# Kernel optimization log

Measured on AMD Instinct MI355X. Metric: run time of the kernel, lower is better.

## Reference

```python
import jax, jax.numpy as jnp
import numpy as np

N_NODES = 100000
D = 128            # hidden_size*2
N_EDGES = 1600000  # avg degree 16
NUM_LABELS = 1024


def setup_inputs() -> dict:
    key = jax.random.key(0)
    ks = jax.random.split(key, 16)
    inputs = jax.random.normal(ks[0], (N_NODES, D), dtype=jnp.float32)
    src = jax.random.randint(ks[1], (N_EDGES,), 0, N_NODES, dtype=jnp.int64)
    dst = jax.random.randint(ks[2], (N_EDGES,), 0, N_NODES, dtype=jnp.int64)
    s = 0.05
    # GIN layer 1 (conv linear) + residual block 1
    eps1 = jnp.zeros((), dtype=jnp.float32)
    W1 = jax.random.normal(ks[3], (D, D), dtype=jnp.float32) * s
    b1 = jnp.zeros((D,), dtype=jnp.float32)
    rW1 = jax.random.normal(ks[4], (D, D), dtype=jnp.float32) * s
    rb1 = jnp.zeros((D,), dtype=jnp.float32)
    # GIN layer 2 + residual block 2
    eps2 = jnp.zeros((), dtype=jnp.float32)
    W2 = jax.random.normal(ks[5], (D, D), dtype=jnp.float32) * s
    b2 = jnp.zeros((D,), dtype=jnp.float32)
    rW2 = jax.random.normal(ks[6], (D, D), dtype=jnp.float32) * s
    rb2 = jnp.zeros((D,), dtype=jnp.float32)
    # final multi-label head
    linW = jax.random.normal(ks[7], (D, NUM_LABELS), dtype=jnp.float32) * s
    linb = jnp.zeros((NUM_LABELS,), dtype=jnp.float32)
    return dict(inputs=inputs, src=src, dst=dst,
                eps1=eps1, W1=W1, b1=b1, rW1=rW1, rb1=rb1,
                eps2=eps2, W2=W2, b2=b2, rW2=rW2, rb2=rb2,
                linW=linW, linb=linb)


def reference(inputs, src, dst, eps1, W1, b1, rW1, rb1,
              eps2, W2, b2, rW2, rb2, linW, linb):
    n = inputs.shape[0]

    def gin_conv(h, eps, W, b):
        # sum-aggregate neighbor features: irregular gather + scatter-add
        agg = jax.ops.segment_sum(h[src], dst, num_segments=n)  # [N, D]
        return ((1.0 + eps) * h + agg) @ W + b

    def residual_block(h, rW, rb):
        # Sequential(ReLU, Dropout(eval=identity), Residual(D, D))
        h = jax.nn.relu(h)
        return h + jax.nn.relu(h @ rW + rb)

    h1 = residual_block(gin_conv(inputs, eps1, W1, b1), rW1, rb1)
    h2 = residual_block(gin_conv(h1, eps2, W2, b2), rW2, rb2)

    stacked = jnp.stack([h1, h2], axis=1)   # [N, n_layers, D] == stack_embed
    pooled = stacked.mean(axis=1)           # [N, D]
    return pooled @ linW + linb             # [N, NUM_LABELS]
```

## Files before the change

### kernel.cpp

```cpp
#include <hip/hip_runtime.h>

#define DIM 128
#define NLAB 1024
#define MT 64
#define LDK 136

typedef __bf16 bf16x4 __attribute__((ext_vector_type(4)));
typedef __bf16 bf16x8 __attribute__((ext_vector_type(8)));
typedef float  f32x4  __attribute__((ext_vector_type(4)));

__global__ __launch_bounds__(256) void k_hist(
    const int* __restrict__ dst, int* __restrict__ cnt, int nE) {
  int e = blockIdx.x * 256 + threadIdx.x;
  if (e < nE) atomicAdd(&cnt[dst[e]], 1);
}

__global__ __launch_bounds__(1024) void k_scan(
    const int* __restrict__ cnt, int* __restrict__ off,
    int* __restrict__ cur, int n) {
  __shared__ int part[1024];
  const int t = threadIdx.x;
  const int per = (n + 1023) >> 10;
  const int start = t * per;
  const int end = min(start + per, n);
  int s = 0;
  for (int i = start; i < end; ++i) s += cnt[i];
  part[t] = s;
  __syncthreads();
  for (int d = 1; d < 1024; d <<= 1) {
    int v = (t >= d) ? part[t - d] : 0;
    __syncthreads();
    part[t] += v;
    __syncthreads();
  }
  int excl = (t == 0) ? 0 : part[t - 1];
  if (t == 1023) off[n] = part[1023];
  for (int i = start; i < end; ++i) {
    int c = cnt[i];
    off[i] = excl;
    cur[i] = excl;
    excl += c;
  }
}

__global__ __launch_bounds__(256) void k_binfill(
    const int* __restrict__ src, const int* __restrict__ dst,
    int* __restrict__ cur, int* __restrict__ eidx, int nE) {
  int e = blockIdx.x * 256 + threadIdx.x;
  if (e < nE) {
    int p = atomicAdd(&cur[dst[e]], 1);
    eidx[p] = src[e];
  }
}

__global__ __launch_bounds__(256) void k_gather(
    const float* __restrict__ h, const int* __restrict__ off,
    const int* __restrict__ eidx, float* __restrict__ agg, int n) {
  int node = blockIdx.x * 8 + (threadIdx.x >> 5);
  if (node >= n) return;
  int c = (threadIdx.x & 31) << 2;
  int beg = off[node], end = off[node + 1];
  float4 a0 = make_float4(0.f, 0.f, 0.f, 0.f);
  float4 a1 = a0, a2 = a0, a3 = a0;
  int e = beg;
  for (; e + 4 <= end; e += 4) {
    int s0 = eidx[e + 0];
    int s1 = eidx[e + 1];
    int s2 = eidx[e + 2];
    int s3 = eidx[e + 3];
    float4 v0 = *(const float4*)(h + (size_t)s0 * DIM + c);
    float4 v1 = *(const float4*)(h + (size_t)s1 * DIM + c);
    float4 v2 = *(const float4*)(h + (size_t)s2 * DIM + c);
    float4 v3 = *(const float4*)(h + (size_t)s3 * DIM + c);
    a0.x += v0.x; a0.y += v0.y; a0.z += v0.z; a0.w += v0.w;
    a1.x += v1.x; a1.y += v1.y; a1.z += v1.z; a1.w += v1.w;
    a2.x += v2.x; a2.y += v2.y; a2.z += v2.z; a2.w += v2.w;
    a3.x += v3.x; a3.y += v3.y; a3.z += v3.z; a3.w += v3.w;
  }
  for (; e < end; ++e) {
    int s = eidx[e];
    float4 v = *(const float4*)(h + (size_t)s * DIM + c);
    a0.x += v.x; a0.y += v.y; a0.z += v.z; a0.w += v.w;
  }
  a0.x += a1.x + a2.x + a3.x;
  a0.y += a1.y + a2.y + a3.y;
  a0.z += a1.z + a2.z + a3.z;
  a0.w += a1.w + a2.w + a3.w;
  *(float4*)(agg + (size_t)node * DIM + c) = a0;
}

__global__ __launch_bounds__(256) void k_gin_conv(
    const float* __restrict__ hin, const float* __restrict__ agg,
    const float* __restrict__ epsp, const float* __restrict__ W,
    const float* __restrict__ bias, float* __restrict__ hout, int n) {
  __shared__ __bf16 As[MT][LDK];
  __shared__ __bf16 Bs[DIM][LDK];
  const int t = threadIdx.x;
  const int rowBase = blockIdx.x * MT;
  const float e1 = 1.0f + epsp[0];

#pragma unroll
  for (int it = 0; it < 8; ++it) {
    int idx = (it * 256 + t) << 2;
    int r = idx >> 7, c = idx & 127;
    int node = rowBase + r;
    float4 a4 = make_float4(0.f, 0.f, 0.f, 0.f);
    float4 g4 = a4;
    if (node < n) {
      a4 = *(const float4*)(hin + (size_t)node * DIM + c);
      g4 = *(const float4*)(agg + (size_t)node * DIM + c);
    }
    bf16x4 v;
    v[0] = (__bf16)(e1 * a4.x + g4.x);
    v[1] = (__bf16)(e1 * a4.y + g4.y);
    v[2] = (__bf16)(e1 * a4.z + g4.z);
    v[3] = (__bf16)(e1 * a4.w + g4.w);
    *(bf16x4*)&As[r][c] = v;
  }
  {
    int nloc = t & 127;
    int kh = (t >> 7) << 6;
#pragma unroll
    for (int kk = 0; kk < 64; ++kk) {
      int k = kh + kk;
      Bs[nloc][k] = (__bf16)W[(size_t)k * DIM + nloc];
    }
  }
  __syncthreads();

  const int wv = t >> 6, lane = t & 63;
  const int quad = lane >> 4, l16 = lane & 15;
  f32x4 acc[4][2];
#pragma unroll
  for (int i = 0; i < 4; ++i) {
    acc[i][0] = f32x4{0.f, 0.f, 0.f, 0.f};
    acc[i][1] = f32x4{0.f, 0.f, 0.f, 0.f};
  }

#pragma unroll
  for (int kc = 0; kc < 4; ++kc) {
    int kb = kc * 32 + quad * 8;
    bf16x8 b0 = *(const bf16x8*)&Bs[wv * 32 + l16][kb];
    bf16x8 b1 = *(const bf16x8*)&Bs[wv * 32 + 16 + l16][kb];
#pragma unroll
    for (int rt = 0; rt < 4; ++rt) {
      bf16x8 a = *(const bf16x8*)&As[rt * 16 + l16][kb];
      acc[rt][0] = __builtin_amdgcn_mfma_f32_16x16x32_bf16(a, b0, acc[rt][0], 0, 0, 0);
      acc[rt][1] = __builtin_amdgcn_mfma_f32_16x16x32_bf16(a, b1, acc[rt][1], 0, 0, 0);
    }
  }

#pragma unroll
  for (int rt = 0; rt < 4; ++rt) {
#pragma unroll
    for (int ct = 0; ct < 2; ++ct) {
      int ncol = wv * 32 + ct * 16 + l16;
      float bv = bias[ncol];
#pragma unroll
      for (int r = 0; r < 4; ++r) {
        int node = rowBase + rt * 16 + quad * 4 + r;
        if (node < n) {
          float v = acc[rt][ct][r] + bv;
          hout[(size_t)node * DIM + ncol] = fmaxf(v, 0.f);
        }
      }
    }
  }
}

__global__ __launch_bounds__(256) void k_residual(
    const float* __restrict__ hmid, const float* __restrict__ W,
    const float* __restrict__ bias, float* __restrict__ hout, int n) {
  __shared__ __bf16 As[MT][LDK];
  __shared__ __bf16 Bs[DIM][LDK];
  const int t = threadIdx.x;
  const int rowBase = blockIdx.x * MT;

#pragma unroll
  for (int it = 0; it < 8; ++it) {
    int idx = (it * 256 + t) << 2;
    int r = idx >> 7, c = idx & 127;
    int node = rowBase + r;
    float4 a4 = make_float4(0.f, 0.f, 0.f, 0.f);
    if (node < n) a4 = *(const float4*)(hmid + (size_t)node * DIM + c);
    bf16x4 v;
    v[0] = (__bf16)a4.x;
    v[1] = (__bf16)a4.y;
    v[2] = (__bf16)a4.z;
    v[3] = (__bf16)a4.w;
    *(bf16x4*)&As[r][c] = v;
  }
  {
    int nloc = t & 127;
    int kh = (t >> 7) << 6;
#pragma unroll
    for (int kk = 0; kk < 64; ++kk) {
      int k = kh + kk;
      Bs[nloc][k] = (__bf16)W[(size_t)k * DIM + nloc];
    }
  }
  __syncthreads();

  const int wv = t >> 6, lane = t & 63;
  const int quad = lane >> 4, l16 = lane & 15;
  f32x4 acc[4][2];
#pragma unroll
  for (int i = 0; i < 4; ++i) {
    acc[i][0] = f32x4{0.f, 0.f, 0.f, 0.f};
    acc[i][1] = f32x4{0.f, 0.f, 0.f, 0.f};
  }

#pragma unroll
  for (int kc = 0; kc < 4; ++kc) {
    int kb = kc * 32 + quad * 8;
    bf16x8 b0 = *(const bf16x8*)&Bs[wv * 32 + l16][kb];
    bf16x8 b1 = *(const bf16x8*)&Bs[wv * 32 + 16 + l16][kb];
#pragma unroll
    for (int rt = 0; rt < 4; ++rt) {
      bf16x8 a = *(const bf16x8*)&As[rt * 16 + l16][kb];
      acc[rt][0] = __builtin_amdgcn_mfma_f32_16x16x32_bf16(a, b0, acc[rt][0], 0, 0, 0);
      acc[rt][1] = __builtin_amdgcn_mfma_f32_16x16x32_bf16(a, b1, acc[rt][1], 0, 0, 0);
    }
  }

#pragma unroll
  for (int rt = 0; rt < 4; ++rt) {
#pragma unroll
    for (int ct = 0; ct < 2; ++ct) {
      int ncol = wv * 32 + ct * 16 + l16;
      float bv = bias[ncol];
#pragma unroll
      for (int r = 0; r < 4; ++r) {
        int node = rowBase + rt * 16 + quad * 4 + r;
        if (node < n) {
          float hv = hmid[(size_t)node * DIM + ncol];
          float v = fmaxf(acc[rt][ct][r] + bv, 0.f);
          hout[(size_t)node * DIM + ncol] = hv + v;
        }
      }
    }
  }
}

__global__ __launch_bounds__(256) void k_final(
    const float* __restrict__ h1, const float* __restrict__ h2,
    const float* __restrict__ W, const float* __restrict__ bias,
    float* __restrict__ out, int n) {
  __shared__ __bf16 As[MT][LDK];
  __shared__ __bf16 Bs[DIM][LDK];
  const int t = threadIdx.x;
  const int rowBase = blockIdx.x * MT;
  const int nb = blockIdx.y << 7;

#pragma unroll
  for (int it = 0; it < 8; ++it) {
    int idx = (it * 256 + t) << 2;
    int r = idx >> 7, c = idx & 127;
    int node = rowBase + r;
    float4 a4 = make_float4(0.f, 0.f, 0.f, 0.f);
    float4 b4 = a4;
    if (node < n) {
      a4 = *(const float4*)(h1 + (size_t)node * DIM + c);
      b4 = *(const float4*)(h2 + (size_t)node * DIM + c);
    }
    bf16x4 v;
    v[0] = (__bf16)(0.5f * (a4.x + b4.x));
    v[1] = (__bf16)(0.5f * (a4.y + b4.y));
    v[2] = (__bf16)(0.5f * (a4.z + b4.z));
    v[3] = (__bf16)(0.5f * (a4.w + b4.w));
    *(bf16x4*)&As[r][c] = v;
  }
  {
    int nloc = t & 127;
    int kh = (t >> 7) << 6;
#pragma unroll
    for (int kk = 0; kk < 64; ++kk) {
      int k = kh + kk;
      Bs[nloc][k] = (__bf16)W[(size_t)k * NLAB + nb + nloc];
    }
  }
  __syncthreads();

  const int wv = t >> 6, lane = t & 63;
  const int quad = lane >> 4, l16 = lane & 15;
  f32x4 acc[4][2];
#pragma unroll
  for (int i = 0; i < 4; ++i) {
    acc[i][0] = f32x4{0.f, 0.f, 0.f, 0.f};
    acc[i][1] = f32x4{0.f, 0.f, 0.f, 0.f};
  }

#pragma unroll
  for (int kc = 0; kc < 4; ++kc) {
    int kb = kc * 32 + quad * 8;
    bf16x8 b0 = *(const bf16x8*)&Bs[wv * 32 + l16][kb];
    bf16x8 b1 = *(const bf16x8*)&Bs[wv * 32 + 16 + l16][kb];
#pragma unroll
    for (int rt = 0; rt < 4; ++rt) {
      bf16x8 a = *(const bf16x8*)&As[rt * 16 + l16][kb];
      acc[rt][0] = __builtin_amdgcn_mfma_f32_16x16x32_bf16(a, b0, acc[rt][0], 0, 0, 0);
      acc[rt][1] = __builtin_amdgcn_mfma_f32_16x16x32_bf16(a, b1, acc[rt][1], 0, 0, 0);
    }
  }

#pragma unroll
  for (int rt = 0; rt < 4; ++rt) {
#pragma unroll
    for (int ct = 0; ct < 2; ++ct) {
      int ncol = wv * 32 + ct * 16 + l16;
      float bv = bias[nb + ncol];
#pragma unroll
      for (int r = 0; r < 4; ++r) {
        int node = rowBase + rt * 16 + quad * 4 + r;
        if (node < n) {
          out[(size_t)node * NLAB + nb + ncol] = acc[rt][ct][r] + bv;
        }
      }
    }
  }
}

extern "C" void kernel_launch(void* const* d_in, const int* in_sizes, int n_in,
                              void* d_out, int out_size, void* d_ws, size_t ws_size,
                              hipStream_t stream) {
  const float* inputs = (const float*)d_in[0];
  const int*   src    = (const int*)d_in[1];
  const int*   dst    = (const int*)d_in[2];
  const float* eps1   = (const float*)d_in[3];
  const float* W1     = (const float*)d_in[4];
  const float* b1     = (const float*)d_in[5];
  const float* rW1    = (const float*)d_in[6];
  const float* rb1    = (const float*)d_in[7];
  const float* eps2   = (const float*)d_in[8];
  const float* W2     = (const float*)d_in[9];
  const float* b2     = (const float*)d_in[10];
  const float* rW2    = (const float*)d_in[11];
  const float* rb2    = (const float*)d_in[12];
  const float* linW   = (const float*)d_in[13];
  const float* linb   = (const float*)d_in[14];
  float* out = (float*)d_out;

  const int n = in_sizes[0] / DIM;
  const int E = in_sizes[1];
  const size_t bufB = (size_t)n * DIM * sizeof(float);

  float* agg  = (float*)d_ws;
  float* hmid = (float*)((char*)d_ws + bufB);
  float* h1   = (float*)((char*)d_ws + 2 * bufB);
  float* h2   = agg;

  int* eidx = (int*)d_out;
  int* off  = eidx + E;
  int* cur  = off + (n + 1);

  const int rowBlocks = (n + MT - 1) / MT;
  const int eBlocks = (E + 255) / 256;
  const int gBlocks = (n + 7) / 8;
  dim3 fgrid(rowBlocks, NLAB / DIM);

  hipMemsetAsync(cur, 0, (size_t)n * sizeof(int), stream);
  k_hist<<<eBlocks, 256, 0, stream>>>(dst, cur, E);
  k_scan<<<1, 1024, 0, stream>>>(cur, off, cur, n);
  k_binfill<<<eBlocks, 256, 0, stream>>>(src, dst, cur, eidx, E);

  k_gather<<<gBlocks, 256, 0, stream>>>(inputs, off, eidx, agg, n);
  k_gin_conv<<<rowBlocks, 256, 0, stream>>>(inputs, agg, eps1, W1, b1, hmid, n);
  k_residual<<<rowBlocks, 256, 0, stream>>>(hmid, rW1, rb1, h1, n);
  k_gather<<<gBlocks, 256, 0, stream>>>(h1, off, eidx, agg, n);
  k_gin_conv<<<rowBlocks, 256, 0, stream>>>(h1, agg, eps2, W2, b2, hmid, n);
  k_residual<<<rowBlocks, 256, 0, stream>>>(hmid, rW2, rb2, h2, n);
  k_final<<<fgrid, 256, 0, stream>>>(h1, h2, linW, linb, out, n);
}
```

Before: 1.387 ms.

## Fuse GIN conv with residual block and fold final head into layer 2

Merges the GIN conv matmul and the residual matmul into one kernel per layer. The intermediate activation stays in registers and LDS instead of a round trip through global memory. Layer 2 also computes the mean of h1 and h2 and loops over all 8 label tiles of the head inside the same block, so h2 is never written. This removes several full-size N×128 reads and writes plus launches. The cost is that each block now loads linW 8 times serially and the final head has less parallelism (one block per row tile instead of 8).

```diff
diff --git a/kernel.cpp b/kernel.cpp
--- a/kernel.cpp
+++ b/kernel.cpp
@@ -89,16 +89,12 @@
   *(float4*)(agg + (size_t)node * DIM + c) = a0;
 }
 
-__global__ __launch_bounds__(256) void k_gin_conv(
-    const float* __restrict__ hin, const float* __restrict__ agg,
-    const float* __restrict__ epsp, const float* __restrict__ W,
-    const float* __restrict__ bias, float* __restrict__ hout, int n) {
-  __shared__ __bf16 As[MT][LDK];
-  __shared__ __bf16 Bs[DIM][LDK];
-  const int t = threadIdx.x;
-  const int rowBase = blockIdx.x * MT;
-  const float e1 = 1.0f + epsp[0];
-
+__device__ __forceinline__ void conv_residual_tile(
+    const float* __restrict__ hin, const float* __restrict__ agg, float e1,
+    const float* __restrict__ W, const float* __restrict__ bias,
+    const float* __restrict__ rW, const float* __restrict__ rbias,
+    __bf16 (*As)[LDK], __bf16 (*Bs)[LDK],
+    int rowBase, int n, int t, float ho[4][2][4]) {
 #pragma unroll
   for (int it = 0; it < 8; ++it) {
     int idx = (it * 256 + t) << 2;
@@ -136,7 +132,6 @@
     acc[i][0] = f32x4{0.f, 0.f, 0.f, 0.f};
     acc[i][1] = f32x4{0.f, 0.f, 0.f, 0.f};
   }
-
 #pragma unroll
   for (int kc = 0; kc < 4; ++kc) {
     int kb = kc * 32 + quad * 8;
@@ -150,173 +145,172 @@
     }
   }
 
-#pragma unroll
-  for (int rt = 0; rt < 4; ++rt) {
-#pragma unroll
-    for (int ct = 0; ct < 2; ++ct) {
-      int ncol = wv * 32 + ct * 16 + l16;
-      float bv = bias[ncol];
-#pragma unroll
-      for (int r = 0; r < 4; ++r) {
-        int node = rowBase + rt * 16 + quad * 4 + r;
-        if (node < n) {
-          float v = acc[rt][ct][r] + bv;
-          hout[(size_t)node * DIM + ncol] = fmaxf(v, 0.f);
-        }
-      }
-    }
-  }
-}
-
-__global__ __launch_bounds__(256) void k_residual(
-    const float* __restrict__ hmid, const float* __restrict__ W,
-    const float* __restrict__ bias, float* __restrict__ hout, int n) {
+  float hm[4][2][4];
+#pragma unroll
+  for (int rt = 0; rt < 4; ++rt)
+#pragma unroll
+    for (int ct = 0; ct < 2; ++ct) {
+      float bv = bias[wv * 32 + ct * 16 + l16];
+#pragma unroll
+      for (int r = 0; r < 4; ++r)
+        hm[rt][ct][r] = fmaxf(acc[rt][ct][r] + bv, 0.f);
+    }
+
+  __syncthreads();
+
+#pragma unroll
+  for (int rt = 0; rt < 4; ++rt)
+#pragma unroll
+    for (int ct = 0; ct < 2; ++ct) {
+      int col = wv * 32 + ct * 16 + l16;
+#pragma unroll
+      for (int r = 0; r < 4; ++r)
+        As[rt * 16 + quad * 4 + r][col] = (__bf16)hm[rt][ct][r];
+    }
+  {
+    int nloc = t & 127;
+    int kh = (t >> 7) << 6;
+#pragma unroll
+    for (int kk = 0; kk < 64; ++kk) {
+      int k = kh + kk;
+      Bs[nloc][k] = (__bf16)rW[(size_t)k * DIM + nloc];
+    }
+  }
+  __syncthreads();
+
+#pragma unroll
+  for (int i = 0; i < 4; ++i) {
+    acc[i][0] = f32x4{0.f, 0.f, 0.f, 0.f};
+    acc[i][1] = f32x4{0.f, 0.f, 0.f, 0.f};
+  }
+#pragma unroll
+  for (int kc = 0; kc < 4; ++kc) {
+    int kb = kc * 32 + quad * 8;
+    bf16x8 b0 = *(const bf16x8*)&Bs[wv * 32 + l16][kb];
+    bf16x8 b1 = *(const bf16x8*)&Bs[wv * 32 + 16 + l16][kb];
+#pragma unroll
+    for (int rt = 0; rt < 4; ++rt) {
+      bf16x8 a = *(const bf16x8*)&As[rt * 16 + l16][kb];
+      acc[rt][0] = __builtin_amdgcn_mfma_f32_16x16x32_bf16(a, b0, acc[rt][0], 0, 0, 0);
+      acc[rt][1] = __builtin_amdgcn_mfma_f32_16x16x32_bf16(a, b1, acc[rt][1], 0, 0, 0);
+    }
+  }
+
+#pragma unroll
+  for (int rt = 0; rt < 4; ++rt)
+#pragma unroll
+    for (int ct = 0; ct < 2; ++ct) {
+      float bv = rbias[wv * 32 + ct * 16 + l16];
+#pragma unroll
+      for (int r = 0; r < 4; ++r)
+        ho[rt][ct][r] = hm[rt][ct][r] + fmaxf(acc[rt][ct][r] + bv, 0.f);
+    }
+}
+
+__global__ __launch_bounds__(256) void k_layer1(
+    const float* __restrict__ hin, const float* __restrict__ agg,
+    const float* __restrict__ epsp, const float* __restrict__ W,
+    const float* __restrict__ bias, const float* __restrict__ rW,
+    const float* __restrict__ rbias, float* __restrict__ h1, int n) {
   __shared__ __bf16 As[MT][LDK];
   __shared__ __bf16 Bs[DIM][LDK];
   const int t = threadIdx.x;
   const int rowBase = blockIdx.x * MT;
-
-#pragma unroll
-  for (int it = 0; it < 8; ++it) {
-    int idx = (it * 256 + t) << 2;
-    int r = idx >> 7, c = idx & 127;
-    int node = rowBase + r;
-    float4 a4 = make_float4(0.f, 0.f, 0.f, 0.f);
-    if (node < n) a4 = *(const float4*)(hmid + (size_t)node * DIM + c);
-    bf16x4 v;
-    v[0] = (__bf16)a4.x;
-    v[1] = (__bf16)a4.y;
-    v[2] = (__bf16)a4.z;
-    v[3] = (__bf16)a4.w;
-    *(bf16x4*)&As[r][c] = v;
-  }
-  {
-    int nloc = t & 127;
-    int kh = (t >> 7) << 6;
-#pragma unroll
-    for (int kk = 0; kk < 64; ++kk) {
-      int k = kh + kk;
-      Bs[nloc][k] = (__bf16)W[(size_t)k * DIM + nloc];
-    }
-  }
-  __syncthreads();
-
+  float ho[4][2][4];
+  conv_residual_tile(hin, agg, 1.0f + epsp[0], W, bias, rW, rbias,
+                     As, Bs, rowBase, n, t, ho);
   const int wv = t >> 6, lane = t & 63;
   const int quad = lane >> 4, l16 = lane & 15;
-  f32x4 acc[4][2];
-#pragma unroll
-  for (int i = 0; i < 4; ++i) {
-    acc[i][0] = f32x4{0.f, 0.f, 0.f, 0.f};
-    acc[i][1] = f32x4{0.f, 0.f, 0.f, 0.f};
-  }
-
-#pragma unroll
-  for (int kc = 0; kc < 4; ++kc) {
-    int kb = kc * 32 + quad * 8;
-    bf16x8 b0 = *(const bf16x8*)&Bs[wv * 32 + l16][kb];
-    bf16x8 b1 = *(const bf16x8*)&Bs[wv * 32 + 16 + l16][kb];
-#pragma unroll
-    for (int rt = 0; rt < 4; ++rt) {
-      bf16x8 a = *(const bf16x8*)&As[rt * 16 + l16][kb];
-      acc[rt][0] = __builtin_amdgcn_mfma_f32_16x16x32_bf16(a, b0, acc[rt][0], 0, 0, 0);
-      acc[rt][1] = __builtin_amdgcn_mfma_f32_16x16x32_bf16(a, b1, acc[rt][1], 0, 0, 0);
-    }
-  }
-
-#pragma unroll
-  for (int rt = 0; rt < 4; ++rt) {
+#pragma unroll
+  for (int rt = 0; rt < 4; ++rt)
 #pragma unroll
     for (int ct = 0; ct < 2; ++ct) {
       int ncol = wv * 32 + ct * 16 + l16;
-      float bv = bias[ncol];
 #pragma unroll
       for (int r = 0; r < 4; ++r) {
         int node = rowBase + rt * 16 + quad * 4 + r;
-        if (node < n) {
-          float hv = hmid[(size_t)node * DIM + ncol];
-          float v = fmaxf(acc[rt][ct][r] + bv, 0.f);
-          hout[(size_t)node * DIM + ncol] = hv + v;
-        }
-      }
-    }
-  }
-}
-
-__global__ __launch_bounds__(256) void k_final(
-    const float* __restrict__ h1, const float* __restrict__ h2,
-    const float* __restrict__ W, const float* __restrict__ bias,
-    float* __restrict__ out, int n) {
+        if (node < n) h1[(size_t)node * DIM + ncol] = ho[rt][ct][r];
+      }
+    }
+}
+
+__global__ __launch_bounds__(256) void k_layer2f(
+    const float* __restrict__ h1, const float* __restrict__ agg,
+    const float* __restrict__ epsp, const float* __restrict__ W,
+    const float* __restrict__ bias, const float* __restrict__ rW,
+    const float* __restrict__ rbias, const float* __restrict__ linW,
+    const float* __restrict__ linb, float* __restrict__ out, int n) {
   __shared__ __bf16 As[MT][LDK];
   __shared__ __bf16 Bs[DIM][LDK];
   const int t = threadIdx.x;
   const int rowBase = blockIdx.x * MT;
-  const int nb = blockIdx.y << 7;
-
-#pragma unroll
-  for (int it = 0; it < 8; ++it) {
-    int idx = (it * 256 + t) << 2;
-    int r = idx >> 7, c = idx & 127;
-    int node = rowBase + r;
-    float4 a4 = make_float4(0.f, 0.f, 0.f, 0.f);
-    float4 b4 = a4;
-    if (node < n) {
-      a4 = *(const float4*)(h1 + (size_t)node * DIM + c);
-      b4 = *(const float4*)(h2 + (size_t)node * DIM + c);
-    }
-    bf16x4 v;
-    v[0] = (__bf16)(0.5f * (a4.x + b4.x));
-    v[1] = (__bf16)(0.5f * (a4.y + b4.y));
-    v[2] = (__bf16)(0.5f * (a4.z + b4.z));
-    v[3] = (__bf16)(0.5f * (a4.w + b4.w));
-    *(bf16x4*)&As[r][c] = v;
-  }
-  {
-    int nloc = t & 127;
-    int kh = (t >> 7) << 6;
-#pragma unroll
-    for (int kk = 0; kk < 64; ++kk) {
-      int k = kh + kk;
-      Bs[nloc][k] = (__bf16)W[(size_t)k * NLAB + nb + nloc];
-    }
-  }
-  __syncthreads();
-
+  float ho[4][2][4];
+  conv_residual_tile(h1, agg, 1.0f + epsp[0], W, bias, rW, rbias,
+                     As, Bs, rowBase, n, t, ho);
   const int wv = t >> 6, lane = t & 63;
   const int quad = lane >> 4, l16 = lane & 15;
-  f32x4 acc[4][2];
-#pragma unroll
-  for (int i = 0; i < 4; ++i) {
-    acc[i][0] = f32x4{0.f, 0.f, 0.f, 0.f};
-    acc[i][1] = f32x4{0.f, 0.f, 0.f, 0.f};
-  }
-
-#pragma unroll
-  for (int kc = 0; kc < 4; ++kc) {
-    int kb = kc * 32 + quad * 8;
-    bf16x8 b0 = *(const bf16x8*)&Bs[wv * 32 + l16][kb];
-    bf16x8 b1 = *(const bf16x8*)&Bs[wv * 32 + 16 + l16][kb];
-#pragma unroll
-    for (int rt = 0; rt < 4; ++rt) {
-      bf16x8 a = *(const bf16x8*)&As[rt * 16 + l16][kb];
-      acc[rt][0] = __builtin_amdgcn_mfma_f32_16x16x32_bf16(a, b0, acc[rt][0], 0, 0, 0);
-      acc[rt][1] = __builtin_amdgcn_mfma_f32_16x16x32_bf16(a, b1, acc[rt][1], 0, 0, 0);
-    }
-  }
-
-#pragma unroll
-  for (int rt = 0; rt < 4; ++rt) {
-#pragma unroll
-    for (int ct = 0; ct < 2; ++ct) {
-      int ncol = wv * 32 + ct * 16 + l16;
-      float bv = bias[nb + ncol];
+
+  __syncthreads();
+
+#pragma unroll
+  for (int rt = 0; rt < 4; ++rt)
+#pragma unroll
+    for (int ct = 0; ct < 2; ++ct) {
+      int col = wv * 32 + ct * 16 + l16;
 #pragma unroll
       for (int r = 0; r < 4; ++r) {
-        int node = rowBase + rt * 16 + quad * 4 + r;
-        if (node < n) {
-          out[(size_t)node * NLAB + nb + ncol] = acc[rt][ct][r] + bv;
+        int lrow = rt * 16 + quad * 4 + r;
+        int node = rowBase + lrow;
+        float h1v = (node < n) ? h1[(size_t)node * DIM + col] : 0.f;
+        As[lrow][col] = (__bf16)(0.5f * (h1v + ho[rt][ct][r]));
+      }
+    }
+
+  for (int nb = 0; nb < 8; ++nb) {
+    int nbase = nb << 7;
+    {
+      int nloc = t & 127;
+      int kh = (t >> 7) << 6;
+#pragma unroll
+      for (int kk = 0; kk < 64; ++kk) {
+        int k = kh + kk;
+        Bs[nloc][k] = (__bf16)linW[(size_t)k * NLAB + nbase + nloc];
+      }
+    }
+    __syncthreads();
+
+    f32x4 acc[4][2];
+#pragma unroll
+    for (int i = 0; i < 4; ++i) {
+      acc[i][0] = f32x4{0.f, 0.f, 0.f, 0.f};
+      acc[i][1] = f32x4{0.f, 0.f, 0.f, 0.f};
+    }
+#pragma unroll
+    for (int kc = 0; kc < 4; ++kc) {
+      int kb = kc * 32 + quad * 8;
+      bf16x8 b0 = *(const bf16x8*)&Bs[wv * 32 + l16][kb];
+      bf16x8 b1 = *(const bf16x8*)&Bs[wv * 32 + 16 + l16][kb];
+#pragma unroll
+      for (int rt = 0; rt < 4; ++rt) {
+        bf16x8 a = *(const bf16x8*)&As[rt * 16 + l16][kb];
+        acc[rt][0] = __builtin_amdgcn_mfma_f32_16x16x32_bf16(a, b0, acc[rt][0], 0, 0, 0);
+        acc[rt][1] = __builtin_amdgcn_mfma_f32_16x16x32_bf16(a, b1, acc[rt][1], 0, 0, 0);
+      }
+    }
+#pragma unroll
+    for (int rt = 0; rt < 4; ++rt)
+#pragma unroll
+      for (int ct = 0; ct < 2; ++ct) {
+        int ncol = wv * 32 + ct * 16 + l16;
+        float bv = linb[nbase + ncol];
+#pragma unroll
+        for (int r = 0; r < 4; ++r) {
+          int node = rowBase + rt * 16 + quad * 4 + r;
+          if (node < n)
+            out[(size_t)node * NLAB + nbase + ncol] = acc[rt][ct][r] + bv;
         }
       }
-    }
+    __syncthreads();
   }
 }
 
@@ -344,10 +338,8 @@
   const int E = in_sizes[1];
   const size_t bufB = (size_t)n * DIM * sizeof(float);
 
-  float* agg  = (float*)d_ws;
-  float* hmid = (float*)((char*)d_ws + bufB);
-  float* h1   = (float*)((char*)d_ws + 2 * bufB);
-  float* h2   = agg;
+  float* agg = (float*)d_ws;
+  float* h1  = (float*)((char*)d_ws + bufB);
 
   int* eidx = (int*)d_out;
   int* off  = eidx + E;
@@ -356,7 +348,6 @@
   const int rowBlocks = (n + MT - 1) / MT;
   const int eBlocks = (E + 255) / 256;
   const int gBlocks = (n + 7) / 8;
-  dim3 fgrid(rowBlocks, NLAB / DIM);
 
   hipMemsetAsync(cur, 0, (size_t)n * sizeof(int), stream);
   k_hist<<<eBlocks, 256, 0, stream>>>(dst, cur, E);
@@ -364,10 +355,8 @@
   k_binfill<<<eBlocks, 256, 0, stream>>>(src, dst, cur, eidx, E);
 
   k_gather<<<gBlocks, 256, 0, stream>>>(inputs, off, eidx, agg, n);
-  k_gin_conv<<<rowBlocks, 256, 0, stream>>>(inputs, agg, eps1, W1, b1, hmid, n);
-  k_residual<<<rowBlocks, 256, 0, stream>>>(hmid, rW1, rb1, h1, n);
+  k_layer1<<<rowBlocks, 256, 0, stream>>>(inputs, agg, eps1, W1, b1, rW1, rb1, h1, n);
   k_gather<<<gBlocks, 256, 0, stream>>>(h1, off, eidx, agg, n);
-  k_gin_conv<<<rowBlocks, 256, 0, stream>>>(h1, agg, eps2, W2, b2, hmid, n);
-  k_residual<<<rowBlocks, 256, 0, stream>>>(hmid, rW2, rb2, h2, n);
-  k_final<<<fgrid, 256, 0, stream>>>(h1, h2, linW, linb, out, n);
-}
+  k_layer2f<<<rowBlocks, 256, 0, stream>>>(h1, agg, eps2, W2, b2, rW2, rb2,
+                                           linW, linb, out, n);
+}
```

After: 1.420 ms. 1.02x slower.
